# Kernel tuning notes

Measured on AMD Instinct MI355X. Metric: run time of the kernel, lower is better.

Reference implementation:

```python
import jax, jax.numpy as jnp
import numpy as np

INV_TEMP = 100.0


def setup_inputs() -> dict:
    key = jax.random.key(0)
    k1, k2, k3 = jax.random.split(key, 3)
    B, C, J, Hh, Wh = 64, 4, 17, 96, 96
    heatmaps = jax.random.normal(k1, (B * C, J, Hh, Wh), dtype=jnp.float32)
    projection_matrices = jax.random.normal(k2, (B, C, 3, 4), dtype=jnp.float32)
    confidences = jax.random.uniform(k3, (B, C, J), dtype=jnp.float32)
    return {
        "heatmaps": heatmaps,
        "projection_matrices": projection_matrices,
        "confidences": confidences,
        "H_img": 384,
        "W_img": 384,
    }


def _softargmax(heatmaps):
    # heatmaps: (B*C, J, Hh, Wh) -> keypoints (B*C, J, 2) as (x, y)
    bc, J, Hh, Wh = heatmaps.shape
    hm = jax.nn.softmax((heatmaps * INV_TEMP).reshape(bc, J, Hh * Wh), axis=-1)
    hm = hm.reshape(bc, J, Hh, Wh)
    xs = jnp.arange(Wh, dtype=hm.dtype)
    ys = jnp.arange(Hh, dtype=hm.dtype)
    kx = jnp.einsum('bjhw,w->bj', hm, xs)  # x = width index (grid c=0)
    ky = jnp.einsum('bjhw,h->bj', hm, ys)  # y = height index (grid c=1)
    return jnp.stack([kx, ky], axis=-1)


def _dlt(P, kp2d, conf):
    # P: (B,C,3,4), kp2d: (B,C,J,2), conf: (B,C,J) -> (B,J,3)
    B, C, J = kp2d.shape[:3]
    # A[b,c,j,i,:] = P[b,c,2,:]*kp2d[b,c,j,i] - P[b,c,i,:], scaled by conf
    A = (P[:, :, None, 2:3, :] * kp2d[:, :, :, :, None]
         - P[:, :, None, :2, :]) * conf[:, :, :, None, None]  # (B,C,J,2,4)
    A = A.transpose(0, 2, 1, 3, 4).reshape(B, J, 2 * C, 4)
    _, _, Vh = jnp.linalg.svd(A, full_matrices=False)  # Vh: (B,J,4,4)
    homo = Vh[..., 3, :]  # smallest right singular vector, (B,J,4)
    return homo[..., :3] / homo[..., 3:4]


def reference(heatmaps, projection_matrices, confidences, H_img, W_img):
    B, C = projection_matrices.shape[:2]
    bc, J, Hh, Wh = heatmaps.shape
    kp = _softargmax(heatmaps)  # (B*C, J, 2)
    # faithful (quirky) rescale: x *= H/Hh, y *= W/Wh as in original code
    scale = jnp.array([H_img / Hh, W_img / Wh], dtype=kp.dtype)
    kp = (kp * scale).reshape(B, C, J, 2)
    return _dlt(projection_matrices, kp, confidences)
```

## Files before the change

kernel.cpp:

```cpp
#include <hip/hip_runtime.h>

#define B_NUM 64
#define C_NUM 4
#define J_NUM 17
#define HH 96
#define WW 96
#define HWSZ (HH * WW)

__device__ __forceinline__ float waveMax(float v) {
#pragma unroll
  for (int o = 32; o > 0; o >>= 1) v = fmaxf(v, __shfl_xor(v, o));
  return v;
}
__device__ __forceinline__ float waveSum(float v) {
#pragma unroll
  for (int o = 32; o > 0; o >>= 1) v += __shfl_xor(v, o);
  return v;
}

__global__ __launch_bounds__(256) void softargmax_k(
    const float* __restrict__ hm, const int* __restrict__ Hp,
    const int* __restrict__ Wp, float* __restrict__ kp) {
  const int r = blockIdx.x;
  const int t = threadIdx.x;
  const float4* row = (const float4*)(hm + (size_t)r * HWSZ);

  float4 v[9];
  float m = -3.4e38f;
#pragma unroll
  for (int k = 0; k < 9; ++k) {
    v[k] = row[k * 256 + t];
    m = fmaxf(m, fmaxf(fmaxf(v[k].x, v[k].y), fmaxf(v[k].z, v[k].w)));
  }
  m = waveMax(m);
  __shared__ float smax[4];
  const int wid = t >> 6, lane = t & 63;
  if (lane == 0) smax[wid] = m;
  __syncthreads();
  m = fmaxf(fmaxf(smax[0], smax[1]), fmaxf(smax[2], smax[3]));
  const float M100 = 100.0f * m;

  float se = 0.f, sx = 0.f, sy = 0.f;
#pragma unroll
  for (int k = 0; k < 9; ++k) {
    const int base = k * 1024 + t * 4;
    const float e0 = __expf(fmaf(100.f, v[k].x, -M100));
    const float e1 = __expf(fmaf(100.f, v[k].y, -M100));
    const float e2 = __expf(fmaf(100.f, v[k].z, -M100));
    const float e3 = __expf(fmaf(100.f, v[k].w, -M100));
    const int h = base / WW;
    const int w0 = base - h * WW;
    const float esum = (e0 + e1) + (e2 + e3);
    se += esum;
    sy += esum * (float)h;
    sx += e0 * (float)w0 + e1 * (float)(w0 + 1) + e2 * (float)(w0 + 2) +
          e3 * (float)(w0 + 3);
  }
  se = waveSum(se);
  sx = waveSum(sx);
  sy = waveSum(sy);
  __shared__ float ssum[4][3];
  if (lane == 0) {
    ssum[wid][0] = se;
    ssum[wid][1] = sx;
    ssum[wid][2] = sy;
  }
  __syncthreads();
  if (t == 0) {
    const float SE = (ssum[0][0] + ssum[1][0]) + (ssum[2][0] + ssum[3][0]);
    const float SX = (ssum[0][1] + ssum[1][1]) + (ssum[2][1] + ssum[3][1]);
    const float SY = (ssum[0][2] + ssum[1][2]) + (ssum[2][2] + ssum[3][2]);
    const float sc_x = (float)Hp[0] / (float)HH;
    const float sc_y = (float)Wp[0] / (float)WW;
    ((float2*)kp)[r] = make_float2(SX / SE * sc_x, SY / SE * sc_y);
  }
}

__global__ __launch_bounds__(256) void dlt_k(
    const float* __restrict__ P, const float* __restrict__ conf,
    const float* __restrict__ kp, float* __restrict__ out) {
  const int idx = blockIdx.x * blockDim.x + threadIdx.x;
  if (idx >= B_NUM * J_NUM) return;
  const int b = idx / J_NUM;
  const int j = idx - b * J_NUM;

  double M[4][4];
#pragma unroll
  for (int a = 0; a < 4; ++a)
#pragma unroll
    for (int bb = 0; bb < 4; ++bb) M[a][bb] = 0.0;

#pragma unroll
  for (int c = 0; c < C_NUM; ++c) {
    const float* Pm = P + ((size_t)(b * C_NUM + c)) * 12;
    const float cf = conf[(b * C_NUM + c) * J_NUM + j];
    const float2 xy = ((const float2*)kp)[(b * C_NUM + c) * J_NUM + j];
    double row0[4], row1[4];
#pragma unroll
    for (int l = 0; l < 4; ++l) {
      const double p2 = (double)Pm[8 + l];
      row0[l] = (p2 * (double)xy.x - (double)Pm[l]) * (double)cf;
      row1[l] = (p2 * (double)xy.y - (double)Pm[4 + l]) * (double)cf;
    }
#pragma unroll
    for (int a = 0; a < 4; ++a)
#pragma unroll
      for (int bb = 0; bb < 4; ++bb)
        M[a][bb] += row0[a] * row0[bb] + row1[a] * row1[bb];
  }

  double V[4][4];
#pragma unroll
  for (int a = 0; a < 4; ++a)
#pragma unroll
    for (int bb = 0; bb < 4; ++bb) V[a][bb] = (a == bb) ? 1.0 : 0.0;

  for (int sweep = 0; sweep < 8; ++sweep) {
#pragma unroll
    for (int p = 0; p < 3; ++p) {
#pragma unroll
      for (int q = p + 1; q < 4; ++q) {
        const double d = M[p][q];
        if (fabs(d) < 1e-300) continue;
        const double a = M[p][p], bq = M[q][q];
        const double theta = (bq - a) / (2.0 * d);
        const double tt =
            (theta >= 0.0 ? 1.0 : -1.0) / (fabs(theta) + sqrt(theta * theta + 1.0));
        const double cc = 1.0 / sqrt(tt * tt + 1.0);
        const double ss = tt * cc;
#pragma unroll
        for (int k = 0; k < 4; ++k) {
          if (k == p || k == q) continue;
          const double mkp = M[k][p], mkq = M[k][q];
          M[k][p] = M[p][k] = cc * mkp - ss * mkq;
          M[k][q] = M[q][k] = ss * mkp + cc * mkq;
        }
        M[p][p] = a - tt * d;
        M[q][q] = bq + tt * d;
        M[p][q] = M[q][p] = 0.0;
#pragma unroll
        for (int k = 0; k < 4; ++k) {
          const double vkp = V[k][p], vkq = V[k][q];
          V[k][p] = cc * vkp - ss * vkq;
          V[k][q] = ss * vkp + cc * vkq;
        }
      }
    }
  }

  int mi = 0;
  double mv = M[0][0];
#pragma unroll
  for (int i = 1; i < 4; ++i)
    if (M[i][i] < mv) { mv = M[i][i]; mi = i; }
  const double h0 = V[0][mi], h1 = V[1][mi], h2 = V[2][mi], h3 = V[3][mi];
  out[idx * 3 + 0] = (float)(h0 / h3);
  out[idx * 3 + 1] = (float)(h1 / h3);
  out[idx * 3 + 2] = (float)(h2 / h3);
}

extern "C" void kernel_launch(void* const* d_in, const int* in_sizes, int n_in,
                              void* d_out, int out_size, void* d_ws, size_t ws_size,
                              hipStream_t stream) {
  const float* hm = (const float*)d_in[0];
  const float* P = (const float*)d_in[1];
  const float* conf = (const float*)d_in[2];
  const int* Hp = (const int*)d_in[3];
  const int* Wp = (const int*)d_in[4];
  float* out = (float*)d_out;
  float* kp = (float*)d_ws;

  softargmax_k<<<B_NUM * C_NUM * J_NUM, 256, 0, stream>>>(hm, Hp, Wp, kp);
  dlt_k<<<(B_NUM * J_NUM + 255) / 256, 256, 0, stream>>>(P, conf, kp, out);
}
```

Before: 239.3 us.

## Fuse softargmax and DLT triangulation into one kernel, one wave per camera

Merges the two kernels so that each block handles one (batch, joint) pair. Each of the four waves reduces one camera's heatmap row, and thread 0 then runs the double-precision Jacobi SVD on the keypoints held in shared memory. This removes the second launch, the workspace round trip and the cross-wave reductions inside the softmax. The costs are 36 float4 registers per lane, a serial fp64 eigen-solve on a single thread at the end of every block, and four times fewer blocks (1088), which may hurt latency hiding on the memory-bound read.

```diff
diff --git a/kernel.cpp b/kernel.cpp
--- a/kernel.cpp
+++ b/kernel.cpp
@@ -18,32 +18,33 @@
   return v;
 }
 
-__global__ __launch_bounds__(256) void softargmax_k(
-    const float* __restrict__ hm, const int* __restrict__ Hp,
-    const int* __restrict__ Wp, float* __restrict__ kp) {
-  const int r = blockIdx.x;
+__global__ __launch_bounds__(256, 1) void triang_fused_k(
+    const float* __restrict__ hm, const float* __restrict__ P,
+    const float* __restrict__ conf, const int* __restrict__ Hp,
+    const int* __restrict__ Wp, float* __restrict__ out) {
+  const int bj = blockIdx.x;
+  const int b = bj / J_NUM;
+  const int j = bj - b * J_NUM;
   const int t = threadIdx.x;
+  const int cam = t >> 6;
+  const int lane = t & 63;
+  const int r = (b * C_NUM + cam) * J_NUM + j;
   const float4* row = (const float4*)(hm + (size_t)r * HWSZ);
 
-  float4 v[9];
+  float4 v[36];
   float m = -3.4e38f;
 #pragma unroll
-  for (int k = 0; k < 9; ++k) {
-    v[k] = row[k * 256 + t];
+  for (int k = 0; k < 36; ++k) {
+    v[k] = row[k * 64 + lane];
     m = fmaxf(m, fmaxf(fmaxf(v[k].x, v[k].y), fmaxf(v[k].z, v[k].w)));
   }
   m = waveMax(m);
-  __shared__ float smax[4];
-  const int wid = t >> 6, lane = t & 63;
-  if (lane == 0) smax[wid] = m;
-  __syncthreads();
-  m = fmaxf(fmaxf(smax[0], smax[1]), fmaxf(smax[2], smax[3]));
   const float M100 = 100.0f * m;
 
   float se = 0.f, sx = 0.f, sy = 0.f;
 #pragma unroll
-  for (int k = 0; k < 9; ++k) {
-    const int base = k * 1024 + t * 4;
+  for (int k = 0; k < 36; ++k) {
+    const int base = k * 256 + lane * 4;
     const float e0 = __expf(fmaf(100.f, v[k].x, -M100));
     const float e1 = __expf(fmaf(100.f, v[k].y, -M100));
     const float e2 = __expf(fmaf(100.f, v[k].z, -M100));
@@ -59,54 +60,41 @@
   se = waveSum(se);
   sx = waveSum(sx);
   sy = waveSum(sy);
-  __shared__ float ssum[4][3];
+
+  __shared__ float skp[C_NUM][2];
   if (lane == 0) {
-    ssum[wid][0] = se;
-    ssum[wid][1] = sx;
-    ssum[wid][2] = sy;
+    const float scx = (float)Hp[0] / (float)HH;
+    const float scy = (float)Wp[0] / (float)WW;
+    skp[cam][0] = sx / se * scx;
+    skp[cam][1] = sy / se * scy;
   }
   __syncthreads();
-  if (t == 0) {
-    const float SE = (ssum[0][0] + ssum[1][0]) + (ssum[2][0] + ssum[3][0]);
-    const float SX = (ssum[0][1] + ssum[1][1]) + (ssum[2][1] + ssum[3][1]);
-    const float SY = (ssum[0][2] + ssum[1][2]) + (ssum[2][2] + ssum[3][2]);
-    const float sc_x = (float)Hp[0] / (float)HH;
-    const float sc_y = (float)Wp[0] / (float)WW;
-    ((float2*)kp)[r] = make_float2(SX / SE * sc_x, SY / SE * sc_y);
-  }
-}
+  if (t != 0) return;
 
-__global__ __launch_bounds__(256) void dlt_k(
-    const float* __restrict__ P, const float* __restrict__ conf,
-    const float* __restrict__ kp, float* __restrict__ out) {
-  const int idx = blockIdx.x * blockDim.x + threadIdx.x;
-  if (idx >= B_NUM * J_NUM) return;
-  const int b = idx / J_NUM;
-  const int j = idx - b * J_NUM;
-
-  double M[4][4];
+  double M4[4][4];
 #pragma unroll
   for (int a = 0; a < 4; ++a)
 #pragma unroll
-    for (int bb = 0; bb < 4; ++bb) M[a][bb] = 0.0;
+    for (int bb = 0; bb < 4; ++bb) M4[a][bb] = 0.0;
 
 #pragma unroll
   for (int c = 0; c < C_NUM; ++c) {
     const float* Pm = P + ((size_t)(b * C_NUM + c)) * 12;
     const float cf = conf[(b * C_NUM + c) * J_NUM + j];
-    const float2 xy = ((const float2*)kp)[(b * C_NUM + c) * J_NUM + j];
+    const double x = (double)skp[c][0];
+    const double y = (double)skp[c][1];
     double row0[4], row1[4];
 #pragma unroll
     for (int l = 0; l < 4; ++l) {
       const double p2 = (double)Pm[8 + l];
-      row0[l] = (p2 * (double)xy.x - (double)Pm[l]) * (double)cf;
-      row1[l] = (p2 * (double)xy.y - (double)Pm[4 + l]) * (double)cf;
+      row0[l] = (p2 * x - (double)Pm[l]) * (double)cf;
+      row1[l] = (p2 * y - (double)Pm[4 + l]) * (double)cf;
     }
 #pragma unroll
     for (int a = 0; a < 4; ++a)
 #pragma unroll
       for (int bb = 0; bb < 4; ++bb)
-        M[a][bb] += row0[a] * row0[bb] + row1[a] * row1[bb];
+        M4[a][bb] += row0[a] * row0[bb] + row1[a] * row1[bb];
   }
 
   double V[4][4];
@@ -120,24 +108,24 @@
     for (int p = 0; p < 3; ++p) {
 #pragma unroll
       for (int q = p + 1; q < 4; ++q) {
-        const double d = M[p][q];
+        const double d = M4[p][q];
         if (fabs(d) < 1e-300) continue;
-        const double a = M[p][p], bq = M[q][q];
+        const double a = M4[p][p], bq = M4[q][q];
         const double theta = (bq - a) / (2.0 * d);
-        const double tt =
-            (theta >= 0.0 ? 1.0 : -1.0) / (fabs(theta) + sqrt(theta * theta + 1.0));
+        const double tt = (theta >= 0.0 ? 1.0 : -1.0) /
+                          (fabs(theta) + sqrt(theta * theta + 1.0));
         const double cc = 1.0 / sqrt(tt * tt + 1.0);
         const double ss = tt * cc;
 #pragma unroll
         for (int k = 0; k < 4; ++k) {
           if (k == p || k == q) continue;
-          const double mkp = M[k][p], mkq = M[k][q];
-          M[k][p] = M[p][k] = cc * mkp - ss * mkq;
-          M[k][q] = M[q][k] = ss * mkp + cc * mkq;
+          const double mkp = M4[k][p], mkq = M4[k][q];
+          M4[k][p] = M4[p][k] = cc * mkp - ss * mkq;
+          M4[k][q] = M4[q][k] = ss * mkp + cc * mkq;
         }
-        M[p][p] = a - tt * d;
-        M[q][q] = bq + tt * d;
-        M[p][q] = M[q][p] = 0.0;
+        M4[p][p] = a - tt * d;
+        M4[q][q] = bq + tt * d;
+        M4[p][q] = M4[q][p] = 0.0;
 #pragma unroll
         for (int k = 0; k < 4; ++k) {
           const double vkp = V[k][p], vkq = V[k][q];
@@ -149,14 +137,14 @@
   }
 
   int mi = 0;
-  double mv = M[0][0];
+  double mv = M4[0][0];
 #pragma unroll
   for (int i = 1; i < 4; ++i)
-    if (M[i][i] < mv) { mv = M[i][i]; mi = i; }
-  const double h0 = V[0][mi], h1 = V[1][mi], h2 = V[2][mi], h3 = V[3][mi];
-  out[idx * 3 + 0] = (float)(h0 / h3);
-  out[idx * 3 + 1] = (float)(h1 / h3);
-  out[idx * 3 + 2] = (float)(h2 / h3);
+    if (M4[i][i] < mv) { mv = M4[i][i]; mi = i; }
+  const double h3 = V[3][mi];
+  out[bj * 3 + 0] = (float)(V[0][mi] / h3);
+  out[bj * 3 + 1] = (float)(V[1][mi] / h3);
+  out[bj * 3 + 2] = (float)(V[2][mi] / h3);
 }
 
 extern "C" void kernel_launch(void* const* d_in, const int* in_sizes, int n_in,
@@ -168,8 +156,6 @@
   const int* Hp = (const int*)d_in[3];
   const int* Wp = (const int*)d_in[4];
   float* out = (float*)d_out;
-  float* kp = (float*)d_ws;
 
-  softargmax_k<<<B_NUM * C_NUM * J_NUM, 256, 0, stream>>>(hm, Hp, Wp, kp);
-  dlt_k<<<(B_NUM * J_NUM + 255) / 256, 256, 0, stream>>>(P, conf, kp, out);
+  triang_fused_k<<<B_NUM * J_NUM, 256, 0, stream>>>(hm, P, conf, Hp, Wp, out);
 }
```

Result: slower. 260.9 us (+9.0%).
